# Performance work log

Hardware: AMD Instinct MI355X
Metric: run time of the kernel (lower is better)

## Reference

```python
import jax, jax.numpy as jnp
import numpy as np

B, S, HID, E, NH, EMB, FFN = 8192, 32, 64, 131072, 8, 64, 64
D = HID // NH  # att_size = 8
SCALE = D ** -0.5
LN_EPS = 1e-5


def _layer_norm(x, g, b):
    m = jnp.mean(x, axis=-1, keepdims=True)
    v = jnp.mean((x - m) ** 2, axis=-1, keepdims=True)
    return (x - m) * jax.lax.rsqrt(v + LN_EPS) * g + b


def setup_inputs() -> dict:
    key = jax.random.key(0)
    ks = jax.random.split(key, 16)
    std = 0.02 / np.sqrt(6.0)  # init_params with n_layers=6

    def w(k, shape):
        return jax.random.normal(k, shape, dtype=jnp.float32) * std

    return {
        "x": jax.random.normal(ks[0], (B, S, HID), dtype=jnp.float32),
        "edge_attr": jax.random.normal(ks[1], (E, EMB), dtype=jnp.float32),
        "edge_index": jax.random.randint(ks[2], (2, E), 0, S),
        "batch": jax.random.randint(ks[3], (B,), 0, B),
        "wq": w(ks[4], (HID, HID)), "bq": jnp.zeros((HID,), jnp.float32),
        "wk": w(ks[5], (HID, HID)), "bk": jnp.zeros((HID,), jnp.float32),
        "wv": w(ks[6], (HID, HID)), "bv": jnp.zeros((HID,), jnp.float32),
        "we": w(ks[7], (EMB, NH)), "be": jnp.zeros((NH,), jnp.float32),
        "wo": w(ks[8], (HID, HID)), "bo": jnp.zeros((HID,), jnp.float32),
        "ln1_g": jnp.ones((HID,), jnp.float32), "ln1_b": jnp.zeros((HID,), jnp.float32),
        "ln2_g": jnp.ones((HID,), jnp.float32), "ln2_b": jnp.zeros((HID,), jnp.float32),
        "w1": w(ks[9], (HID, FFN)), "b1": jnp.zeros((FFN,), jnp.float32),
        "w2": w(ks[10], (FFN, HID)), "b2": jnp.zeros((HID,), jnp.float32),
    }


def reference(x, edge_attr, edge_index, batch, wq, bq, wk, bk, wv, bv,
              we, be, wo, bo, ln1_g, ln1_b, ln2_g, ln2_b, w1, b1, w2, b2):
    # --- EncoderLayer.forward (eval mode: dropout = identity) ---
    y = _layer_norm(x, ln1_g, ln1_b)

    # MultiHeadAttention: project and split heads -> [B, NH, S, D]
    def heads(t, w_, b_):
        return (t @ w_ + b_).reshape(B, S, NH, D).transpose(0, 2, 1, 3)

    q = heads(y, wq, bq)
    k = heads(y, wk, bk)
    v = heads(y, wv, bv)

    # Sparse edge bias scattered into dense [B, NH, S, S] scores
    edge_weights = edge_attr @ we + be                      # [E, NH]
    src, dst = edge_index[0], edge_index[1]
    graph_id = batch[src]                                   # [E]
    edge_bias = jnp.zeros((B, NH, S, S), dtype=x.dtype)
    edge_bias = edge_bias.at[graph_id, :, src, dst].add(edge_weights)

    scores = jnp.einsum("bhsd,bhtd->bhst", q * SCALE, k) + edge_bias
    attn = jax.nn.softmax(scores, axis=-1)
    out = jnp.einsum("bhst,bhtd->bhsd", attn, v)            # [B, NH, S, D]
    out = out.transpose(0, 2, 1, 3).reshape(B, S, HID)
    out = out @ wo + bo

    x = x + out

    # FFN block
    z = _layer_norm(x, ln2_g, ln2_b)
    z = jax.nn.gelu(z @ w1 + b1, approximate=False) @ w2 + b2
    return x + z
```

## Files before the change

### kernel.cpp

```cpp
#include <hip/hip_runtime.h>

#define NB 8192
#define SS 32
#define NEDGE 131072
#define GPB 16
#define ITERS (GPB / 2)
#define EB 256
#define EPB (NEDGE / EB)
#define ATT_SCALE 0.35355339059327373f
#define LN_EPS 1e-5f

typedef const float* __restrict__ cfp;
typedef __attribute__((ext_vector_type(8))) short bfrag;
typedef __attribute__((ext_vector_type(4))) float f32x4;

__device__ inline short f2bf(float f) {
  union { float f; unsigned u; } un; un.f = f;
  unsigned r = un.u + 0x7FFFu + ((un.u >> 16) & 1u);
  return (short)(r >> 16);
}
__device__ inline float bf2f(short s) {
  union { unsigned u; float f; } un;
  un.u = ((unsigned)(unsigned short)s) << 16;
  return un.f;
}
__device__ inline unsigned cvt_pk(float lo, float hi) {
  unsigned r;
  asm("v_cvt_pk_bf16_f32 %0, %1, %2" : "=v"(r) : "v"(lo), "v"(hi));
  return r;
}
__device__ inline bfrag pack8(const float* y) {
  union { uint4 u4; bfrag b; } c;
  c.u4.x = cvt_pk(y[0], y[1]); c.u4.y = cvt_pk(y[2], y[3]);
  c.u4.z = cvt_pk(y[4], y[5]); c.u4.w = cvt_pk(y[6], y[7]);
  return c.b;
}
__device__ inline int lad(int row, int col) {
  return row * 64 + (((col >> 3) ^ (row & 7)) * 8) + (col & 7);
}

__global__ __launch_bounds__(256) void edge_partial_kernel(
    cfp edge_attr, const int* __restrict__ edge_index, cfp we, cfp be,
    float* __restrict__ Wpart) {
  __shared__ float Wl[8 * SS * SS];
  const int t = threadIdx.x;
  const int lane = t & 63, w = t >> 6;
  const int g = lane >> 4, r = lane & 15;
  for (int i = t; i < 8 * SS * SS; i += 256) Wl[i] = 0.f;

  bfrag b0 = {0,0,0,0,0,0,0,0}, b1 = b0;
  float beh = 0.f;
  if (r < 8) {
#pragma unroll
    for (int j = 0; j < 8; ++j) {
      b0[j] = f2bf(we[(g * 8 + j) * 8 + r]);
      b1[j] = f2bf(we[(32 + g * 8 + j) * 8 + r]);
    }
    beh = be[r];
  }
  __syncthreads();

  const f32x4 zero4 = {0.f, 0.f, 0.f, 0.f};
  for (int itr = 0; itr < EPB / 64; ++itr) {
    const int e0 = blockIdx.x * EPB + itr * 64 + w * 16;
    const float* src = edge_attr + (long)(e0 + r) * 64;
    float va[8], vb[8];
    *(float4*)&va[0] = *(const float4*)(src + g * 8);
    *(float4*)&va[4] = *(const float4*)(src + g * 8 + 4);
    *(float4*)&vb[0] = *(const float4*)(src + 32 + g * 8);
    *(float4*)&vb[4] = *(const float4*)(src + 32 + g * 8 + 4);
    bfrag a0 = pack8(va), a1 = pack8(vb);
    f32x4 c = zero4;
    c = __builtin_amdgcn_mfma_f32_16x16x32_bf16(a0, b0, c, 0, 0, 0);
    c = __builtin_amdgcn_mfma_f32_16x16x32_bf16(a1, b1, c, 0, 0, 0);
    if (r < 8) {
#pragma unroll
      for (int j = 0; j < 4; ++j) {
        const int eg = e0 + g * 4 + j;
        const int s = edge_index[eg];
        const int d = edge_index[NEDGE + eg];
        atomicAdd(&Wl[(r * SS + s) * SS + d], c[j] + beh);
      }
    }
  }
  __syncthreads();
  const float4* Wl4 = (const float4*)Wl;
  float4* dst = (float4*)(Wpart + (long)blockIdx.x * 8192);
  for (int i = t; i < 2048; i += 256) dst[i] = Wl4[i];
}

__global__ __launch_bounds__(256) void edge_reduce_kernel(
    cfp Wpart, float* __restrict__ W) {
  __shared__ float4 accs[8][32];
  const int t = threadIdx.x;
  const int slot = blockIdx.x * 32 + (t & 31);
  const int grp = t >> 5;
  float4 s = make_float4(0.f, 0.f, 0.f, 0.f);
#pragma unroll 4
  for (int p = grp * 32; p < grp * 32 + 32; ++p) {
    float4 v = ((const float4*)Wpart)[(long)p * 2048 + slot];
    s.x += v.x; s.y += v.y; s.z += v.z; s.w += v.w;
  }
  accs[grp][t & 31] = s;
  __syncthreads();
  if (t < 32) {
    float4 a = accs[0][t];
#pragma unroll
    for (int q = 1; q < 8; ++q) {
      float4 v = accs[q][t];
      a.x += v.x; a.y += v.y; a.z += v.z; a.w += v.w;
    }
    ((float4*)W)[blockIdx.x * 32 + t] = a;
  }
}

__global__ __launch_bounds__(512, 4) void encoder_kernel(
    cfp x, const int* __restrict__ batch,
    cfp wq, cfp bq, cfp wk, cfp bk, cfp wv, cfp bv, cfp wo, cfp bo,
    cfp ln1g, cfp ln1b, cfp ln2g, cfp ln2b,
    cfp w1, cfp bf1, cfp w2, cfp bf2,
    cfp W, float* __restrict__ out) {

  __shared__ short wt[6][64 * 64];
  __shared__ short P[64 * 64], Q[64 * 64], R[64 * 64];
  __shared__ float bias_s[10][64];
  __shared__ int batch_s[SS];

  const int t = threadIdx.x;

  {
    const int n = t & 63, kb = (t >> 6) * 8;
    auto stage = [&](cfp src, short* dst) {
      bfrag p;
#pragma unroll
      for (int j = 0; j < 8; ++j) p[j] = f2bf(src[(kb + j) * 64 + n]);
      *(bfrag*)&dst[lad(n, kb)] = p;
    };
    stage(wq, wt[0]); stage(wk, wt[1]); stage(wv, wt[2]);
    stage(wo, wt[3]); stage(w1, wt[4]); stage(w2, wt[5]);
  }
  if (t < 64) {
    bias_s[0][t] = bq[t];   bias_s[1][t] = bk[t];   bias_s[2][t] = bv[t];
    bias_s[3][t] = bo[t];   bias_s[4][t] = bf1[t];  bias_s[5][t] = bf2[t];
    bias_s[6][t] = ln1g[t]; bias_s[7][t] = ln1b[t];
    bias_s[8][t] = ln2g[t]; bias_s[9][t] = ln2b[t];
  }
  if (t < SS) batch_s[t] = batch[t];
  __syncthreads();

  const int lane = t & 63, w = t >> 6;
  const int g = lane >> 4, r = lane & 15;
  const int tr = w >> 1, tc0 = (w & 1) * 2;
  const int s8 = t >> 3, c8 = (t & 7) * 8;
  const int gW = w >> 2, hb = (w & 3) * 2;
  const f32x4 zero4 = {0.f, 0.f, 0.f, 0.f};

  auto mm2 = [&](const short* A, const short* Wm, f32x4 acc[2]) {
    const int rr = tr * 16 + r;
    bfrag a0 = *(const bfrag*)&A[lad(rr, g * 8)];
    bfrag a1 = *(const bfrag*)&A[lad(rr, 32 + g * 8)];
#pragma unroll
    for (int i = 0; i < 2; ++i) {
      const int n = (tc0 + i) * 16 + r;
      bfrag b0 = *(const bfrag*)&Wm[lad(n, g * 8)];
      bfrag b1 = *(const bfrag*)&Wm[lad(n, 32 + g * 8)];
      acc[i] = __builtin_amdgcn_mfma_f32_16x16x32_bf16(a0, b0, acc[i], 0, 0, 0);
      acc[i] = __builtin_amdgcn_mfma_f32_16x16x32_bf16(a1, b1, acc[i], 0, 0, 0);
    }
  };

  for (int it = 0; it < ITERS; ++it) {
    const int giter = blockIdx.x * GPB + it * 2;

    {
      float xv[8];
      const float4* px = (const float4*)(x + ((long)(giter * 32 + s8)) * 64 + c8);
      float4 a = px[0], c = px[1];
      xv[0]=a.x; xv[1]=a.y; xv[2]=a.z; xv[3]=a.w;
      xv[4]=c.x; xv[5]=c.y; xv[6]=c.z; xv[7]=c.w;
      float sum = 0.f;
#pragma unroll
      for (int i = 0; i < 8; ++i) sum += xv[i];
      sum += __shfl_xor(sum, 1); sum += __shfl_xor(sum, 2); sum += __shfl_xor(sum, 4);
      const float m = sum * (1.f / 64.f);
      float sq = 0.f;
#pragma unroll
      for (int i = 0; i < 8; ++i) { float dd = xv[i] - m; sq += dd * dd; }
      sq += __shfl_xor(sq, 1); sq += __shfl_xor(sq, 2); sq += __shfl_xor(sq, 4);
      const float rs = rsqrtf(sq * (1.f / 64.f) + LN_EPS);
      bfrag yv;
#pragma unroll
      for (int i = 0; i < 8; ++i)
        yv[i] = f2bf((xv[i] - m) * rs * bias_s[6][c8 + i] + bias_s[7][c8 + i]);
      *(bfrag*)&P[lad(s8, c8)] = yv;
    }
    __syncthreads();

    {
      const int rr = tr * 16 + r;
      bfrag a0 = *(const bfrag*)&P[lad(rr, g * 8)];
      bfrag a1 = *(const bfrag*)&P[lad(rr, 32 + g * 8)];
      f32x4 acc[3][2];
#pragma unroll
      for (int m = 0; m < 3; ++m) { acc[m][0] = zero4; acc[m][1] = zero4; }
#pragma unroll
      for (int i = 0; i < 2; ++i) {
        const int n = (tc0 + i) * 16 + r;
#pragma unroll
        for (int m = 0; m < 3; ++m) {
          bfrag b0 = *(const bfrag*)&wt[m][lad(n, g * 8)];
          bfrag b1 = *(const bfrag*)&wt[m][lad(n, 32 + g * 8)];
          acc[m][i] = __builtin_amdgcn_mfma_f32_16x16x32_bf16(a0, b0, acc[m][i], 0, 0, 0);
          acc[m][i] = __builtin_amdgcn_mfma_f32_16x16x32_bf16(a1, b1, acc[m][i], 0, 0, 0);
        }
      }
#pragma unroll
      for (int i = 0; i < 2; ++i) {
        const int col = (tc0 + i) * 16 + r;
        const float bq_ = bias_s[0][col], bk_ = bias_s[1][col];
#pragma unroll
        for (int j = 0; j < 4; ++j) {
          const int row = tr * 16 + g * 4 + j;
          const int ad = lad(row, col);
          Q[ad] = f2bf((acc[0][i][j] + bq_) * ATT_SCALE);
          R[ad] = f2bf(acc[1][i][j] + bk_);
        }
      }
      __syncthreads();
#pragma unroll
      for (int i = 0; i < 2; ++i) {
        const int hd = (tc0 + i) * 16 + r;
        const float bv_ = bias_s[2][hd];
        const int graph = tr >> 1;
        const int tgrp = (tr & 1) * 2 + (g >> 1);
        unsigned p0 = cvt_pk(acc[2][i][0] + bv_, acc[2][i][1] + bv_);
        unsigned p1 = cvt_pk(acc[2][i][2] + bv_, acc[2][i][3] + bv_);
        const int ad = graph * 2048 + hd * 32 + ((tgrp ^ (hd & 3)) * 8) + (g & 1) * 4;
        *(unsigned*)&P[ad] = p0;
        *(unsigned*)&P[ad + 2] = p1;
      }
    }
    __syncthreads();

    {
      const int gidx2 = giter + gW;
#pragma unroll
      for (int u = 0; u < 2; ++u) {
        const int h = hb + u;
        bfrag kf0 = {0,0,0,0,0,0,0,0}, kf1 = kf0;
        if (g == 0) {
          kf0 = *(const bfrag*)&R[lad(gW * 32 + r, h * 8)];
          kf1 = *(const bfrag*)&R[lad(gW * 32 + 16 + r, h * 8)];
        }
#pragma unroll
        for (int st = 0; st < 2; ++st) {
          const int sL = st * 16 + r;
          bfrag qf = {0,0,0,0,0,0,0,0};
          if (g == 0) qf = *(const bfrag*)&Q[lad(gW * 32 + sL, h * 8)];
          f32x4 sc0 = zero4, sc1 = zero4;
          sc0 = __builtin_amdgcn_mfma_f32_16x16x32_bf16(kf0, qf, sc0, 0, 0, 0);
          sc1 = __builtin_amdgcn_mfma_f32_16x16x32_bf16(kf1, qf, sc1, 0, 0, 0);
          f32x4 wb0 = zero4, wb1 = zero4;
          if (batch_s[sL] == gidx2) {
            wb0 = *(const f32x4*)&W[(h * 32 + sL) * 32 + 4 * g];
            wb1 = *(const f32x4*)&W[(h * 32 + sL) * 32 + 16 + 4 * g];
          }
          float v0[4], v1[4];
#pragma unroll
          for (int j = 0; j < 4; ++j) { v0[j] = sc0[j] + wb0[j]; v1[j] = sc1[j] + wb1[j]; }
          float mx = fmaxf(fmaxf(fmaxf(v0[0], v0[1]), fmaxf(v0[2], v0[3])),
                           fmaxf(fmaxf(v1[0], v1[1]), fmaxf(v1[2], v1[3])));
          mx = fmaxf(mx, __shfl_xor(mx, 16));
          mx = fmaxf(mx, __shfl_xor(mx, 32));
          float e0[4], e1[4], ssum = 0.f;
#pragma unroll
          for (int j = 0; j < 4; ++j) {
            e0[j] = __expf(v0[j] - mx); e1[j] = __expf(v1[j] - mx);
            ssum += e0[j] + e1[j];
          }
          ssum += __shfl_xor(ssum, 16);
          ssum += __shfl_xor(ssum, 32);
          const float inv = __builtin_amdgcn_rcpf(ssum);
          unsigned u0 = cvt_pk(e0[0], e0[1]), u1 = cvt_pk(e0[2], e0[3]);
          unsigned u2 = cvt_pk(e1[0], e1[1]), u3 = cvt_pk(e1[2], e1[3]);
          const int srcA = ((g & 1) * 2) * 16 + r, srcB = srcA + 16;
          unsigned A0 = (unsigned)__shfl((int)u0, srcA);
          unsigned A2 = (unsigned)__shfl((int)u2, srcA);
          unsigned B0 = (unsigned)__shfl((int)u1, srcA);
          unsigned B2 = (unsigned)__shfl((int)u3, srcA);
          unsigned C0 = (unsigned)__shfl((int)u0, srcB);
          unsigned C2 = (unsigned)__shfl((int)u2, srcB);
          unsigned D0 = (unsigned)__shfl((int)u1, srcB);
          unsigned D2 = (unsigned)__shfl((int)u3, srcB);
          const bool hi = (g >> 1);
          uint4 bw;
          bw.x = hi ? A2 : A0;
          bw.y = hi ? B2 : B0;
          bw.z = hi ? C2 : C0;
          bw.w = hi ? D2 : D0;
          bfrag pb = *(bfrag*)&bw;
          bfrag vf = {0,0,0,0,0,0,0,0};
          if (r < 8) {
            const int hd = h * 8 + r;
            vf = *(const bfrag*)&P[gW * 2048 + hd * 32 + ((g ^ (hd & 3)) * 8)];
          }
          f32x4 o = zero4;
          o = __builtin_amdgcn_mfma_f32_16x16x32_bf16(vf, pb, o, 0, 0, 0);
          if (g < 2) {
            unsigned w0 = cvt_pk(o[0] * inv, o[1] * inv);
            unsigned w1 = cvt_pk(o[2] * inv, o[3] * inv);
            const int row = gW * 32 + sL;
            const int ad = lad(row, h * 8) + g * 4;
            *(unsigned*)&Q[ad] = w0;
            *(unsigned*)&Q[ad + 2] = w1;
          }
        }
      }
    }
    __syncthreads();

    f32x4 rx[2];
    {
      f32x4 acc[2] = {zero4, zero4};
      mm2(Q, wt[3], acc);
#pragma unroll
      for (int i = 0; i < 2; ++i) {
        const int col = (tc0 + i) * 16 + r;
        const float bb = bias_s[3][col];
#pragma unroll
        for (int j = 0; j < 4; ++j) {
          const int row = tr * 16 + g * 4 + j;
          const float xv = x[((long)(giter * 32 + row)) * 64 + col];
          const float v = acc[i][j] + bb + xv;
          rx[i][j] = v;
          R[lad(row, col)] = f2bf(v);
        }
      }
    }
    __syncthreads();

    {
      bfrag xv8 = *(const bfrag*)&R[lad(s8, c8)];
      float zv[8];
#pragma unroll
      for (int i = 0; i < 8; ++i) zv[i] = bf2f(xv8[i]);
      float sum = 0.f;
#pragma unroll
      for (int i = 0; i < 8; ++i) sum += zv[i];
      sum += __shfl_xor(sum, 1); sum += __shfl_xor(sum, 2); sum += __shfl_xor(sum, 4);
      const float m = sum * (1.f / 64.f);
      float sq = 0.f;
#pragma unroll
      for (int i = 0; i < 8; ++i) { float dd = zv[i] - m; sq += dd * dd; }
      sq += __shfl_xor(sq, 1); sq += __shfl_xor(sq, 2); sq += __shfl_xor(sq, 4);
      const float rs = rsqrtf(sq * (1.f / 64.f) + LN_EPS);
      bfrag zb;
#pragma unroll
      for (int i = 0; i < 8; ++i)
        zb[i] = f2bf((zv[i] - m) * rs * bias_s[8][c8 + i] + bias_s[9][c8 + i]);
      *(bfrag*)&P[lad(s8, c8)] = zb;
    }
    __syncthreads();

    {
      f32x4 acc[2] = {zero4, zero4};
      mm2(P, wt[4], acc);
#pragma unroll
      for (int i = 0; i < 2; ++i) {
        const int col = (tc0 + i) * 16 + r;
        const float bb = bias_s[4][col];
#pragma unroll
        for (int j = 0; j < 4; ++j) {
          const int row = tr * 16 + g * 4 + j;
          const float u_ = acc[i][j] + bb;
          const float z = -1.5957691216f * (u_ + 0.044715f * u_ * u_ * u_);
          Q[lad(row, col)] = f2bf(u_ * __builtin_amdgcn_rcpf(1.f + __expf(z)));
        }
      }
    }
    __syncthreads();

    {
      f32x4 acc[2] = {zero4, zero4};
      mm2(Q, wt[5], acc);
#pragma unroll
      for (int i = 0; i < 2; ++i) {
        const int col = (tc0 + i) * 16 + r;
        const float bb = bias_s[5][col];
#pragma unroll
        for (int j = 0; j < 4; ++j) {
          const int row = tr * 16 + g * 4 + j;
          out[((long)(giter * 32 + row)) * 64 + col] = acc[i][j] + bb + rx[i][j];
        }
      }
    }
  }
}

extern "C" void kernel_launch(void* const* d_in, const int* in_sizes, int n_in,
                              void* d_out, int out_size, void* d_ws, size_t ws_size,
                              hipStream_t stream) {
  (void)in_sizes; (void)n_in; (void)out_size; (void)ws_size;
  cfp x         = (cfp)d_in[0];
  cfp edge_attr = (cfp)d_in[1];
  const int* edge_index = (const int*)d_in[2];
  const int* batch      = (const int*)d_in[3];
  cfp wq = (cfp)d_in[4];  cfp bq = (cfp)d_in[5];
  cfp wk = (cfp)d_in[6];  cfp bk = (cfp)d_in[7];
  cfp wv = (cfp)d_in[8];  cfp bv = (cfp)d_in[9];
  cfp we = (cfp)d_in[10]; cfp be = (cfp)d_in[11];
  cfp wo = (cfp)d_in[12]; cfp bo = (cfp)d_in[13];
  cfp ln1g = (cfp)d_in[14]; cfp ln1b = (cfp)d_in[15];
  cfp ln2g = (cfp)d_in[16]; cfp ln2b = (cfp)d_in[17];
  cfp w1 = (cfp)d_in[18]; cfp bf1 = (cfp)d_in[19];
  cfp w2 = (cfp)d_in[20]; cfp bf2 = (cfp)d_in[21];
  float* out = (float*)d_out;
  float* W = (float*)d_ws;
  float* Wpart = (float*)d_out;

  edge_partial_kernel<<<EB, 256, 0, stream>>>(edge_attr, edge_index, we, be, Wpart);
  edge_reduce_kernel<<<64, 256, 0, stream>>>(Wpart, W);
  encoder_kernel<<<NB / GPB, 512, 0, stream>>>(x, batch,
      wq, bq, wk, bk, wv, bv, wo, bo,
      ln1g, ln1b, ln2g, ln2b, w1, bf1, w2, bf2, W, out);
}
```

Measured before the change: 97.10 us.

## Fuse LN2 into FFN1 operand registers and prefetch next LN1 early

LN2 is now computed directly in MFMA A-fragment layout. Each lane reduces across its two 8-element row fragments with lane shuffles, so the normalized row goes straight into registers and the LDS round trip plus one barrier are removed. LN1 for the next graph pair is software-pipelined: it runs right after the output projection of the current iteration, sharing that barrier, and one extra barrier is added at the end of the loop. This cuts barriers per iteration and overlaps the x loads with compute. In exchange, each thread does twice the LN2 reduction work, and P must not be overwritten before FFN1 has read it.

```diff
diff --git a/kernel.cpp b/kernel.cpp
--- a/kernel.cpp
+++ b/kernel.cpp
@@ -146,7 +146,6 @@
     bias_s[8][t] = ln2g[t]; bias_s[9][t] = ln2b[t];
   }
   if (t < SS) batch_s[t] = batch[t];
-  __syncthreads();
 
   const int lane = t & 63, w = t >> 6;
   const int g = lane >> 4, r = lane & 15;
@@ -169,32 +168,35 @@
     }
   };
 
+  auto ln1_phase = [&](int gbase) {
+    float xv[8];
+    const float4* px = (const float4*)(x + ((long)(gbase * 32 + s8)) * 64 + c8);
+    float4 a = px[0], c = px[1];
+    xv[0]=a.x; xv[1]=a.y; xv[2]=a.z; xv[3]=a.w;
+    xv[4]=c.x; xv[5]=c.y; xv[6]=c.z; xv[7]=c.w;
+    float sum = 0.f;
+#pragma unroll
+    for (int i = 0; i < 8; ++i) sum += xv[i];
+    sum += __shfl_xor(sum, 1); sum += __shfl_xor(sum, 2); sum += __shfl_xor(sum, 4);
+    const float m = sum * (1.f / 64.f);
+    float sq = 0.f;
+#pragma unroll
+    for (int i = 0; i < 8; ++i) { float dd = xv[i] - m; sq += dd * dd; }
+    sq += __shfl_xor(sq, 1); sq += __shfl_xor(sq, 2); sq += __shfl_xor(sq, 4);
+    const float rs = rsqrtf(sq * (1.f / 64.f) + LN_EPS);
+    bfrag yv;
+#pragma unroll
+    for (int i = 0; i < 8; ++i)
+      yv[i] = f2bf((xv[i] - m) * rs * bias_s[6][c8 + i] + bias_s[7][c8 + i]);
+    *(bfrag*)&P[lad(s8, c8)] = yv;
+  };
+
+  __syncthreads();
+  ln1_phase(blockIdx.x * GPB);
+  __syncthreads();
+
   for (int it = 0; it < ITERS; ++it) {
     const int giter = blockIdx.x * GPB + it * 2;
-
-    {
-      float xv[8];
-      const float4* px = (const float4*)(x + ((long)(giter * 32 + s8)) * 64 + c8);
-      float4 a = px[0], c = px[1];
-      xv[0]=a.x; xv[1]=a.y; xv[2]=a.z; xv[3]=a.w;
-      xv[4]=c.x; xv[5]=c.y; xv[6]=c.z; xv[7]=c.w;
-      float sum = 0.f;
-#pragma unroll
-      for (int i = 0; i < 8; ++i) sum += xv[i];
-      sum += __shfl_xor(sum, 1); sum += __shfl_xor(sum, 2); sum += __shfl_xor(sum, 4);
-      const float m = sum * (1.f / 64.f);
-      float sq = 0.f;
-#pragma unroll
-      for (int i = 0; i < 8; ++i) { float dd = xv[i] - m; sq += dd * dd; }
-      sq += __shfl_xor(sq, 1); sq += __shfl_xor(sq, 2); sq += __shfl_xor(sq, 4);
-      const float rs = rsqrtf(sq * (1.f / 64.f) + LN_EPS);
-      bfrag yv;
-#pragma unroll
-      for (int i = 0; i < 8; ++i)
-        yv[i] = f2bf((xv[i] - m) * rs * bias_s[6][c8 + i] + bias_s[7][c8 + i]);
-      *(bfrag*)&P[lad(s8, c8)] = yv;
-    }
-    __syncthreads();
 
     {
       const int rr = tr * 16 + r;
@@ -337,34 +339,55 @@
         }
       }
     }
+    if (it + 1 < ITERS) ln1_phase(giter + 2);
     __syncthreads();
 
     {
-      bfrag xv8 = *(const bfrag*)&R[lad(s8, c8)];
-      float zv[8];
-#pragma unroll
-      for (int i = 0; i < 8; ++i) zv[i] = bf2f(xv8[i]);
+      const int rr = tr * 16 + r;
+      bfrag z0 = *(const bfrag*)&R[lad(rr, g * 8)];
+      bfrag z1 = *(const bfrag*)&R[lad(rr, 32 + g * 8)];
+      float za[8], zb[8];
+#pragma unroll
+      for (int i = 0; i < 8; ++i) { za[i] = bf2f(z0[i]); zb[i] = bf2f(z1[i]); }
       float sum = 0.f;
 #pragma unroll
-      for (int i = 0; i < 8; ++i) sum += zv[i];
-      sum += __shfl_xor(sum, 1); sum += __shfl_xor(sum, 2); sum += __shfl_xor(sum, 4);
+      for (int i = 0; i < 8; ++i) sum += za[i] + zb[i];
+      sum += __shfl_xor(sum, 16); sum += __shfl_xor(sum, 32);
       const float m = sum * (1.f / 64.f);
       float sq = 0.f;
 #pragma unroll
-      for (int i = 0; i < 8; ++i) { float dd = zv[i] - m; sq += dd * dd; }
-      sq += __shfl_xor(sq, 1); sq += __shfl_xor(sq, 2); sq += __shfl_xor(sq, 4);
+      for (int i = 0; i < 8; ++i) {
+        float d0 = za[i] - m, d1 = zb[i] - m;
+        sq += d0 * d0 + d1 * d1;
+      }
+      sq += __shfl_xor(sq, 16); sq += __shfl_xor(sq, 32);
       const float rs = rsqrtf(sq * (1.f / 64.f) + LN_EPS);
-      bfrag zb;
-#pragma unroll
-      for (int i = 0; i < 8; ++i)
-        zb[i] = f2bf((zv[i] - m) * rs * bias_s[8][c8 + i] + bias_s[9][c8 + i]);
-      *(bfrag*)&P[lad(s8, c8)] = zb;
-    }
-    __syncthreads();
-
-    {
+      float ga[8], gb[8], ba[8], bb2[8];
+      *(float4*)&ga[0]  = *(const float4*)(bias_s[8] + g * 8);
+      *(float4*)&ga[4]  = *(const float4*)(bias_s[8] + g * 8 + 4);
+      *(float4*)&gb[0]  = *(const float4*)(bias_s[8] + 32 + g * 8);
+      *(float4*)&gb[4]  = *(const float4*)(bias_s[8] + 32 + g * 8 + 4);
+      *(float4*)&ba[0]  = *(const float4*)(bias_s[9] + g * 8);
+      *(float4*)&ba[4]  = *(const float4*)(bias_s[9] + g * 8 + 4);
+      *(float4*)&bb2[0] = *(const float4*)(bias_s[9] + 32 + g * 8);
+      *(float4*)&bb2[4] = *(const float4*)(bias_s[9] + 32 + g * 8 + 4);
+      float ya[8], yb2[8];
+#pragma unroll
+      for (int i = 0; i < 8; ++i) {
+        ya[i]  = (za[i] - m) * rs * ga[i] + ba[i];
+        yb2[i] = (zb[i] - m) * rs * gb[i] + bb2[i];
+      }
+      bfrag a0 = pack8(ya), a1 = pack8(yb2);
+
       f32x4 acc[2] = {zero4, zero4};
-      mm2(P, wt[4], acc);
+#pragma unroll
+      for (int i = 0; i < 2; ++i) {
+        const int n = (tc0 + i) * 16 + r;
+        bfrag b0 = *(const bfrag*)&wt[4][lad(n, g * 8)];
+        bfrag b1 = *(const bfrag*)&wt[4][lad(n, 32 + g * 8)];
+        acc[i] = __builtin_amdgcn_mfma_f32_16x16x32_bf16(a0, b0, acc[i], 0, 0, 0);
+        acc[i] = __builtin_amdgcn_mfma_f32_16x16x32_bf16(a1, b1, acc[i], 0, 0, 0);
+      }
 #pragma unroll
       for (int i = 0; i < 2; ++i) {
         const int col = (tc0 + i) * 16 + r;
@@ -394,6 +417,7 @@
         }
       }
     }
+    __syncthreads();
   }
 }
 
```

New measurement: 149.7 us. 54.2% more time.
